# Optimization experiments

Measured on AMD Instinct MI355X. Metric: run time of the kernel, lower is better.

## Reference

```python
import jax, jax.numpy as jnp
import numpy as np

# dims: B=batch, S=src_len, H=hidden, E=char_embed, V=vocab, L=lstm layers
B, S, H, E, V, L = 512, 64, 1024, 256, 128, 2


def setup_inputs() -> dict:
    key = jax.random.key(0)
    ks = jax.random.split(key, 20)
    def n(k, shape, scale=0.05):
        return jax.random.normal(k, shape, dtype=jnp.float32) * scale
    return {
        "input_ids": jax.random.randint(ks[0], (B, 1), 0, V),
        "hidden": n(ks[1], (L, B, H), 1.0),
        "cell": n(ks[2], (L, B, H), 1.0),
        "encoder_outputs": n(ks[3], (B, S, H), 1.0),
        "emb": n(ks[4], (V, E)),          # nn.Embedding weight
        "U": n(ks[5], (H, H)),             # attention U (applied as x @ U)
        "W": n(ks[6], (H, H)),             # attention W
        "Vw": n(ks[7], (H, 1)),            # attention V -> scalar score
        "Wih0": n(ks[8], (4 * H, E + H)),  # LSTM layer0 input weights (i,f,g,o)
        "Whh0": n(ks[9], (4 * H, H)),
        "bih0": n(ks[10], (4 * H,)),
        "bhh0": n(ks[11], (4 * H,)),
        "Wih1": n(ks[12], (4 * H, H)),     # LSTM layer1
        "Whh1": n(ks[13], (4 * H, H)),
        "bih1": n(ks[14], (4 * H,)),
        "bhh1": n(ks[15], (4 * H,)),
        "out_w": n(ks[16], (V, H)),        # output nn.Linear weight (out,in)
        "out_b": n(ks[17], (V,)),
        "matrix": 0,
    }


def _lstm_step(x, h, c, Wih, Whh, bih, bhh):
    g = x @ Wih.T + h @ Whh.T + bih + bhh          # (B, 4H), torch gate order i,f,g,o
    i, f, gg, o = jnp.split(g, 4, axis=-1)
    c2 = jax.nn.sigmoid(f) * c + jax.nn.sigmoid(i) * jnp.tanh(gg)
    h2 = jax.nn.sigmoid(o) * jnp.tanh(c2)
    return h2, c2


def reference(input_ids, hidden, cell, encoder_outputs, emb, U, W, Vw,
              Wih0, Whh0, bih0, bhh0, Wih1, Whh1, bih1, bhh1,
              out_w, out_b, matrix):
    embedded = emb[input_ids]                                  # (B,1,E)
    t1 = jnp.einsum('bsh,hk->bsk', encoder_outputs, U)         # U(enc): (B,S,H)
    t2 = hidden[-1] @ W                                        # W(h_top): (B,H)
    e = jnp.tanh(t1 + t2[:, None, :]) @ Vw                     # scores: (B,S,1)
    a = jax.nn.softmax(e, axis=1)                              # attention weights over S
    ct = jnp.einsum('bso,bsh->boh', a, encoder_outputs)        # context: (B,1,H)
    x = jnp.concatenate([embedded, ct], axis=2)[:, 0, :]       # (B, E+H); dropout p=0 -> identity
    h0, c0 = _lstm_step(x, hidden[0], cell[0], Wih0, Whh0, bih0, bhh0)
    h1, c1 = _lstm_step(h0, hidden[1], cell[1], Wih1, Whh1, bih1, bhh1)
    out = (h1 @ out_w.T + out_b)[:, None, :]                   # (B,1,V)
    h_new = jnp.stack([h0, h1])
    c_new = jnp.stack([c0, c1])
    if matrix:
        return (a, out, h_new, c_new)
    return (out, h_new, c_new)
```

## Files before the change

### kernel.cpp

```cpp
#include <hip/hip_runtime.h>
#include <stdint.h>

#define BB 512
#define SS 64
#define HH 1024
#define EE 256
#define VV 128

typedef __attribute__((ext_vector_type(8))) short bf16x8;
typedef __attribute__((ext_vector_type(4))) float f32x4;

constexpr size_t OFF_ENC   = 0;
constexpr size_t OFF_WIH0  = OFF_ENC   + 67108864UL;
constexpr size_t OFF_WHH0  = OFF_WIH0  + 10485760UL;
constexpr size_t OFF_WIH1  = OFF_WHH0  + 8388608UL;
constexpr size_t OFF_WHH1  = OFF_WIH1  + 8388608UL;
constexpr size_t OFF_OUTW  = OFF_WHH1  + 8388608UL;
constexpr size_t OFF_HID0  = OFF_OUTW  + 262144UL;
constexpr size_t OFF_HLAST = OFF_HID0  + 1048576UL;
constexpr size_t OFF_UT    = OFF_HLAST + 1048576UL;
constexpr size_t OFF_WT    = OFF_UT    + 2097152UL;
constexpr size_t OFF_T2    = OFF_WT    + 2097152UL;
constexpr size_t OFF_E     = OFF_T2    + 2097152UL;
constexpr size_t OFF_EMB   = OFF_E     + 131072UL;
constexpr size_t OFF_CT    = OFF_EMB   + 262144UL;
constexpr size_t OFF_G     = OFF_CT    + 1048576UL;
constexpr size_t OFF_H0B   = OFF_G     + 8388608UL;
constexpr size_t OFF_H1B   = OFF_H0B   + 1048576UL;

__device__ __forceinline__ unsigned short f2bf(float f) {
  unsigned int u = __float_as_uint(f);
  unsigned int r = (u + 0x7FFFu + ((u >> 16) & 1u)) >> 16;
  return (unsigned short)r;
}
__device__ __forceinline__ float bf2f(unsigned short h) {
  return __uint_as_float(((unsigned int)h) << 16);
}

__device__ __forceinline__ void gload_lds16(const void* g, void* l) {
  __builtin_amdgcn_global_load_lds(
      (const __attribute__((address_space(1))) unsigned int*)g,
      (__attribute__((address_space(3))) unsigned int*)l, 16, 0, 0);
}

__global__ void cvt_all(const float* __restrict__ enc, const float* __restrict__ Wih0,
                        const float* __restrict__ Whh0, const float* __restrict__ Wih1,
                        const float* __restrict__ Whh1, const float* __restrict__ outw,
                        const float* __restrict__ hid, char* __restrict__ ws) {
  long i = (long)blockIdx.x * 256 + threadIdx.x;
  const long stride = (long)gridDim.x * 256;
  for (; i < 13139968L; i += stride) {
    const float4* src; ushort4* dst; long j;
    if (i < 8388608L)       { src = (const float4*)enc;  dst = (ushort4*)(ws + OFF_ENC);  j = i; }
    else if (i < 9699328L)  { src = (const float4*)Wih0; dst = (ushort4*)(ws + OFF_WIH0); j = i - 8388608L; }
    else if (i < 10747904L) { src = (const float4*)Whh0; dst = (ushort4*)(ws + OFF_WHH0); j = i - 9699328L; }
    else if (i < 11796480L) { src = (const float4*)Wih1; dst = (ushort4*)(ws + OFF_WIH1); j = i - 10747904L; }
    else if (i < 12845056L) { src = (const float4*)Whh1; dst = (ushort4*)(ws + OFF_WHH1); j = i - 11796480L; }
    else if (i < 12877824L) { src = (const float4*)outw; dst = (ushort4*)(ws + OFF_OUTW); j = i - 12845056L; }
    else if (i < 13008896L) { src = (const float4*)hid;  dst = (ushort4*)(ws + OFF_HID0); j = i - 12877824L; }
    else { src = (const float4*)(hid + 524288); dst = (ushort4*)(ws + OFF_HLAST); j = i - 13008896L; }
    float4 v = src[j];
    ushort4 o;
    o.x = f2bf(v.x); o.y = f2bf(v.y); o.z = f2bf(v.z); o.w = f2bf(v.w);
    dst[j] = o;
  }
}

__global__ void transpose_cvt2(const float* __restrict__ U, const float* __restrict__ W,
                               char* __restrict__ ws) {
  __shared__ float tile[32][33];
  const float* in = blockIdx.z ? W : U;
  unsigned short* out = (unsigned short*)(ws + (blockIdx.z ? OFF_WT : OFF_UT));
  int bc = blockIdx.x * 32, br = blockIdx.y * 32;
  int tx = threadIdx.x & 31, ty = threadIdx.x >> 5;
#pragma unroll
  for (int i = 0; i < 32; i += 8)
    tile[ty + i][tx] = in[(long)(br + ty + i) * HH + bc + tx];
  __syncthreads();
#pragma unroll
  for (int i = 0; i < 32; i += 8)
    out[(long)(bc + ty + i) * HH + br + tx] = f2bf(tile[tx][ty + i]);
}

__global__ void build_xemb(const int* __restrict__ ids, const float* __restrict__ emb,
                           unsigned short* __restrict__ embb) {
  int t = blockIdx.x * 256 + threadIdx.x;
  int b = t >> 6, c4 = t & 63;
  float4 v = ((const float4*)(emb + (long)ids[b] * 256))[c4];
  ushort4 o;
  o.x = f2bf(v.x); o.y = f2bf(v.y); o.z = f2bf(v.z); o.w = f2bf(v.w);
  ((ushort4*)embb)[t] = o;
}

__global__ __launch_bounds__(256) void gemm_seg(
    const unsigned short* __restrict__ A0, int KA0,
    const unsigned short* __restrict__ A1, int KA1,
    const unsigned short* __restrict__ A2,
    const unsigned short* __restrict__ B0, int KB0,
    const unsigned short* __restrict__ B1,
    float* __restrict__ C, int N, int Ktot) {
  __shared__ alignas(128) unsigned short lA[128 * 64];
  __shared__ alignas(128) unsigned short lB[64 * 64];
  const int tid = threadIdx.x;
  const int lane = tid & 63, wid = tid >> 6;
  const int wr = wid >> 1, wc = wid & 1;
  const int fr = lane & 15, fg = lane >> 4;
  f32x4 acc[4][2] = {};
  const long rowA0 = (long)blockIdx.x * 128;
  const long rowB0 = (long)blockIdx.y * 64;
  for (int kt = 0; kt < Ktot; kt += 64) {
    const unsigned short* Ap; int ka, lda;
    if (kt < KA0)            { Ap = A0; ka = kt;             lda = KA0; }
    else if (kt < KA0 + KA1) { Ap = A1; ka = kt - KA0;       lda = KA1; }
    else                     { Ap = A2; ka = kt - KA0 - KA1; lda = 1024; }
    const unsigned short* Bp; int kb, ldb;
    if (kt < KB0) { Bp = B0; kb = kt;       ldb = KB0; }
    else          { Bp = B1; kb = kt - KB0; ldb = 1024; }
#pragma unroll
    for (int j = 0; j < 4; ++j) {
      int c = j * 256 + tid;
      int r = c >> 3, cc = c & 7;
      int sc = cc ^ ((r >> 1) & 7);
      gload_lds16(Ap + (rowA0 + r) * (long)lda + ka + sc * 8, &lA[c * 8]);
    }
#pragma unroll
    for (int j = 0; j < 2; ++j) {
      int c = j * 256 + tid;
      int r = c >> 3, cc = c & 7;
      int sc = cc ^ ((r >> 1) & 7);
      gload_lds16(Bp + (rowB0 + r) * (long)ldb + kb + sc * 8, &lB[c * 8]);
    }
    __syncthreads();
#pragma unroll
    for (int kk = 0; kk < 64; kk += 32) {
      bf16x8 af[4], bfv[2];
#pragma unroll
      for (int m = 0; m < 4; ++m) {
        int row = wr * 64 + m * 16 + fr;
        int ch = ((kk >> 3) + fg) ^ ((row >> 1) & 7);
        af[m] = *(const bf16x8*)&lA[row * 64 + ch * 8];
      }
#pragma unroll
      for (int n = 0; n < 2; ++n) {
        int row = wc * 32 + n * 16 + fr;
        int ch = ((kk >> 3) + fg) ^ ((row >> 1) & 7);
        bfv[n] = *(const bf16x8*)&lB[row * 64 + ch * 8];
      }
#pragma unroll
      for (int m = 0; m < 4; ++m)
#pragma unroll
        for (int n = 0; n < 2; ++n)
          acc[m][n] = __builtin_amdgcn_mfma_f32_16x16x32_bf16(af[m], bfv[n],
                                                              acc[m][n], 0, 0, 0);
    }
    __syncthreads();
  }
#pragma unroll
  for (int m = 0; m < 4; ++m)
#pragma unroll
    for (int n = 0; n < 2; ++n)
#pragma unroll
      for (int r = 0; r < 4; ++r) {
        long grow = rowA0 + wr * 64 + m * 16 + fg * 4 + r;
        long gcol = rowB0 + wc * 32 + n * 16 + fr;
        C[grow * N + gcol] = acc[m][n][r];
      }
}

__global__ __launch_bounds__(256) void gemm_outproj(
    const unsigned short* __restrict__ A, const unsigned short* __restrict__ Bt,
    float* __restrict__ C) {
  __shared__ alignas(128) unsigned short lA[128 * 64];
  __shared__ alignas(128) unsigned short lB[128 * 64];
  const int tid = threadIdx.x;
  const int lane = tid & 63, wid = tid >> 6;
  const int wr = wid >> 1, wc = wid & 1;
  const int fr = lane & 15, fg = lane >> 4;
  f32x4 acc[4][4] = {};
  const long rowA0 = (long)blockIdx.x * 128;
  const int k0 = blockIdx.y * 128;
  for (int kt = k0; kt < k0 + 128; kt += 64) {
#pragma unroll
    for (int j = 0; j < 4; ++j) {
      int c = j * 256 + tid;
      int r = c >> 3, cc = c & 7;
      gload_lds16(A + (rowA0 + r) * 1024 + kt + cc * 8, &lA[c * 8]);
    }
#pragma unroll
    for (int j = 0; j < 4; ++j) {
      int c = j * 256 + tid;
      int r = c >> 3, cc = c & 7;
      gload_lds16(Bt + (long)r * 1024 + kt + cc * 8, &lB[c * 8]);
    }
    __syncthreads();
#pragma unroll
    for (int kk = 0; kk < 64; kk += 32) {
      bf16x8 af[4], bfv[4];
#pragma unroll
      for (int m = 0; m < 4; ++m)
        af[m] = *(const bf16x8*)&lA[(wr * 64 + m * 16 + fr) * 64 + kk + fg * 8];
#pragma unroll
      for (int n = 0; n < 4; ++n)
        bfv[n] = *(const bf16x8*)&lB[(wc * 64 + n * 16 + fr) * 64 + kk + fg * 8];
#pragma unroll
      for (int m = 0; m < 4; ++m)
#pragma unroll
        for (int n = 0; n < 4; ++n)
          acc[m][n] = __builtin_amdgcn_mfma_f32_16x16x32_bf16(af[m], bfv[n],
                                                              acc[m][n], 0, 0, 0);
    }
    __syncthreads();
  }
#pragma unroll
  for (int m = 0; m < 4; ++m)
#pragma unroll
    for (int n = 0; n < 4; ++n)
#pragma unroll
      for (int r = 0; r < 4; ++r) {
        long grow = rowA0 + wr * 64 + m * 16 + fg * 4 + r;
        long gcol = wc * 64 + n * 16 + fr;
        atomicAdd(&C[grow * 128 + gcol], acc[m][n][r]);
      }
}

__global__ void init_out_bias(const float* __restrict__ ob, float* __restrict__ out) {
  int i = blockIdx.x * 256 + threadIdx.x;
  out[i] = ob[i & 127];
}

__global__ __launch_bounds__(512, 2) void gemm_score256(
    const unsigned short* __restrict__ A, const unsigned short* __restrict__ Bt,
    const float* __restrict__ t2, const float* __restrict__ Vw,
    float* __restrict__ e) {
  extern __shared__ unsigned short smem[];
  const int K = HH;
  const int tid = threadIdx.x;
  const int lane = tid & 63, wid = tid >> 6;
  const int wr = wid >> 2;
  const int wcc = wid & 3;
  const int fr = lane & 15, fg = lane >> 4;
  int flat = blockIdx.y * 4 + blockIdx.x;
  int swz = (flat & 7) * 64 + (flat >> 3);
  const long rowA0 = (long)(swz >> 2) * 256;
  const long rowB0 = (long)(swz & 3) * 256;
  const int NKT = 16, NIT = 8;

  f32x4 acc[8][4] = {};

  auto RA = [&](int buf, int kh) { return (const unsigned short*)(smem + (buf * 4 + kh * 2) * 8192); };
  auto RB = [&](int buf, int kh) { return (const unsigned short*)(smem + (buf * 4 + kh * 2 + 1) * 8192); };

  auto stage = [&](int buf, int reg, int ktile) {
    const unsigned short* base = (reg & 1) ? Bt : A;
    long r0 = (reg & 1) ? rowB0 : rowA0;
    int kb = ktile * 64 + (reg >> 1) * 32;
    unsigned short* dst = smem + (buf * 4 + reg) * 8192;
#pragma unroll
    for (int j = 0; j < 2; ++j) {
      int c = j * 512 + tid;
      int row = c >> 2;
      int fgl = (c & 3) ^ ((row >> 1) & 3);
      gload_lds16(base + (r0 + row) * (long)K + kb + fgl * 8, dst + c * 8);
    }
  };
  auto readA = [&](const unsigned short* rg, int mh, bf16x8* af) {
#pragma unroll
    for (int m = 0; m < 4; ++m) {
      int row = wr * 128 + mh * 64 + m * 16 + fr;
      int slot = fg ^ ((row >> 1) & 3);
      af[m] = *(const bf16x8*)(rg + row * 32 + slot * 8);
    }
  };
  auto readB = [&](const unsigned short* rg, bf16x8* bv) {
#pragma unroll
    for (int n = 0; n < 4; ++n) {
      int row = wcc * 64 + n * 16 + fr;
      int slot = fg ^ ((row >> 1) & 3);
      bv[n] = *(const bf16x8*)(rg + row * 32 + slot * 8);
    }
  };
  auto mfma16 = [&](int mh, const bf16x8* af, const bf16x8* bv) {
    __builtin_amdgcn_s_setprio(1);
#pragma unroll
    for (int m = 0; m < 4; ++m)
#pragma unroll
      for (int n = 0; n < 4; ++n)
        acc[mh * 4 + m][n] = __builtin_amdgcn_mfma_f32_16x16x32_bf16(
            af[m], bv[n], acc[mh * 4 + m][n], 0, 0, 0);
    __builtin_amdgcn_s_setprio(0);
  };

#define BAR() __builtin_amdgcn_s_barrier()
#define WAIT6() asm volatile("s_waitcnt vmcnt(6)" ::: "memory")

  bf16x8 afA[4], afB[4], bvA[4], bvB[4];

  stage(0, 0, 0); stage(0, 1, 0); stage(0, 2, 0); stage(0, 3, 0);
  stage(1, 0, 1); stage(1, 1, 1);
  asm volatile("s_waitcnt vmcnt(8)" ::: "memory");
  BAR();
  readA(RA(0, 0), 0, afA); readB(RB(0, 0), bvA);

  for (int t = 0; t < NIT; ++t) {
    int k1 = 2 * t + 1, k2 = 2 * t + 2, k3 = 2 * t + 3;
    if (k2 >= NKT) k2 -= NKT;
    if (k3 >= NKT) k3 -= NKT;
    readA(RA(0, 0), 1, afB);
    stage(1, 2, k1);
    BAR(); mfma16(0, afA, bvA); BAR();
    WAIT6();
    readA(RA(0, 1), 0, afA); readB(RB(0, 1), bvB);
    stage(1, 3, k1);
    BAR(); mfma16(1, afB, bvA); BAR();
    readA(RA(0, 1), 1, afB);
    stage(0, 0, k2);
    BAR(); mfma16(0, afA, bvB); BAR();
    WAIT6();
    readA(RA(1, 0), 0, afA); readB(RB(1, 0), bvA);
    stage(0, 1, k2);
    BAR(); mfma16(1, afB, bvB); BAR();
    readA(RA(1, 0), 1, afB);
    stage(0, 2, k2);
    BAR(); mfma16(0, afA, bvA); BAR();
    WAIT6();
    readA(RA(1, 1), 0, afA); readB(RB(1, 1), bvB);
    stage(0, 3, k2);
    BAR(); mfma16(1, afB, bvA); BAR();
    readA(RA(1, 1), 1, afB);
    stage(1, 0, k3);
    BAR(); mfma16(0, afA, bvB); BAR();
    WAIT6();
    readA(RA(0, 0), 0, afA); readB(RB(0, 0), bvA);
    stage(1, 1, k3);
    BAR(); mfma16(1, afB, bvB); BAR();
  }
  asm volatile("s_waitcnt vmcnt(0)" ::: "memory");

  float t2v[2][4], vw[4];
#pragma unroll
  for (int n = 0; n < 4; ++n) {
    long col = rowB0 + wcc * 64 + n * 16 + fr;
    vw[n] = Vw[col];
#pragma unroll
    for (int h = 0; h < 2; ++h) {
      long b = (rowA0 >> 6) + wr * 2 + h;
      t2v[h][n] = t2[b * HH + col];
    }
  }
#pragma unroll
  for (int i = 0; i < 8; ++i) {
    int hsel = i >> 2;
    float part[4] = {0.f, 0.f, 0.f, 0.f};
#pragma unroll
    for (int n = 0; n < 4; ++n) {
#pragma unroll
      for (int r = 0; r < 4; ++r) {
        float tval = acc[i][n][r] + t2v[hsel][n];
        float th = 1.f - 2.f / (__expf(2.f * tval) + 1.f);
        part[r] += th * vw[n];
      }
    }
#pragma unroll
    for (int r = 0; r < 4; ++r) {
      float p = part[r];
      p += __shfl_xor(p, 1);
      p += __shfl_xor(p, 2);
      p += __shfl_xor(p, 4);
      p += __shfl_xor(p, 8);
      if (fr == 0)
        atomicAdd(&e[rowA0 + wr * 128 + i * 16 + fg * 4 + r], p);
    }
  }
#undef BAR
#undef WAIT6
}

__global__ void softmax_ctx(const float* __restrict__ e,
                            const unsigned short* __restrict__ encb,
                            unsigned short* __restrict__ ctb) {
  __shared__ float als[2][64];
  const int tid = threadIdx.x;
  const int bpair = blockIdx.x;
  if (tid < 128) {
    int b = bpair * 2 + (tid >> 6), s = tid & 63;
    float v = e[b * 64 + s];
    float mx = v;
#pragma unroll
    for (int o = 32; o; o >>= 1) mx = fmaxf(mx, __shfl_xor(mx, o));
    float ex = __expf(v - mx);
    float sm = ex;
#pragma unroll
    for (int o = 32; o; o >>= 1) sm += __shfl_xor(sm, o);
    als[tid >> 6][s] = ex / sm;
  }
  __syncthreads();
  int bi = tid >> 7, hg = tid & 127;
  int b = bpair * 2 + bi;
  const unsigned short* er = encb + (long)b * (SS * HH) + hg * 8;
  float s[8] = {0.f, 0.f, 0.f, 0.f, 0.f, 0.f, 0.f, 0.f};
  for (int i = 0; i < 64; ++i) {
    float av = als[bi][i];
    bf16x8 v = *(const bf16x8*)(er + (long)i * HH);
#pragma unroll
    for (int j = 0; j < 8; ++j) s[j] += av * bf2f((unsigned short)v[j]);
  }
  unsigned short* dst = ctb + (long)b * HH + hg * 8;
#pragma unroll
  for (int j = 0; j < 8; ++j) dst[j] = f2bf(s[j]);
}

__global__ void lstm_cell(const float* __restrict__ g, const float* __restrict__ bih,
                          const float* __restrict__ bhh, const float* __restrict__ cin,
                          float* __restrict__ hout, float* __restrict__ cout,
                          unsigned short* __restrict__ hb) {
  int idx = blockIdx.x * 256 + threadIdx.x;
  int b = idx >> 10, h = idx & 1023;
  const float* gr = g + (long)b * 4096;
  float gi = gr[h] + bih[h] + bhh[h];
  float gf = gr[1024 + h] + bih[1024 + h] + bhh[1024 + h];
  float gg = gr[2048 + h] + bih[2048 + h] + bhh[2048 + h];
  float go = gr[3072 + h] + bih[3072 + h] + bhh[3072 + h];
  float si = 1.f / (1.f + __expf(-gi));
  float sf = 1.f / (1.f + __expf(-gf));
  float so = 1.f / (1.f + __expf(-go));
  float tg = 1.f - 2.f / (__expf(2.f * gg) + 1.f);
  float c2 = sf * cin[idx] + si * tg;
  float tc = 1.f - 2.f / (__expf(2.f * c2) + 1.f);
  float h2 = so * tc;
  cout[idx] = c2;
  hout[idx] = h2;
  hb[idx] = f2bf(h2);
}

extern "C" void kernel_launch(void* const* d_in, const int* in_sizes, int n_in,
                              void* d_out, int out_size, void* d_ws, size_t ws_size,
                              hipStream_t stream) {
  const int* ids = (const int*)d_in[0];
  const float* hidden = (const float*)d_in[1];
  const float* cell = (const float*)d_in[2];
  const float* enc = (const float*)d_in[3];
  const float* emb = (const float*)d_in[4];
  const float* U = (const float*)d_in[5];
  const float* W = (const float*)d_in[6];
  const float* Vw = (const float*)d_in[7];
  const float* Wih0 = (const float*)d_in[8];
  const float* Whh0 = (const float*)d_in[9];
  const float* bih0 = (const float*)d_in[10];
  const float* bhh0 = (const float*)d_in[11];
  const float* Wih1 = (const float*)d_in[12];
  const float* Whh1 = (const float*)d_in[13];
  const float* bih1 = (const float*)d_in[14];
  const float* bhh1 = (const float*)d_in[15];
  const float* out_w = (const float*)d_in[16];
  const float* out_b = (const float*)d_in[17];
  float* out = (float*)d_out;
  char* ws = (char*)d_ws;
  (void)in_sizes; (void)n_in; (void)out_size; (void)ws_size;

  unsigned short* enc_b  = (unsigned short*)(ws + OFF_ENC);
  unsigned short* Wih0b  = (unsigned short*)(ws + OFF_WIH0);
  unsigned short* Whh0b  = (unsigned short*)(ws + OFF_WHH0);
  unsigned short* Wih1b  = (unsigned short*)(ws + OFF_WIH1);
  unsigned short* Whh1b  = (unsigned short*)(ws + OFF_WHH1);
  unsigned short* outwb  = (unsigned short*)(ws + OFF_OUTW);
  unsigned short* hid0b  = (unsigned short*)(ws + OFF_HID0);
  unsigned short* hlastb = (unsigned short*)(ws + OFF_HLAST);
  unsigned short* Utb    = (unsigned short*)(ws + OFF_UT);
  unsigned short* Wtb    = (unsigned short*)(ws + OFF_WT);
  float*          t2     = (float*)(ws + OFF_T2);
  float*          e      = (float*)(ws + OFF_E);
  unsigned short* embb   = (unsigned short*)(ws + OFF_EMB);
  unsigned short* ctb    = (unsigned short*)(ws + OFF_CT);
  float*          g      = (float*)(ws + OFF_G);
  unsigned short* h0b    = (unsigned short*)(ws + OFF_H0B);
  unsigned short* h1b    = (unsigned short*)(ws + OFF_H1B);

  float* out_logits = out;
  float* h_new = out + BB * VV;
  float* c_new = h_new + 2 * BB * HH;

  cvt_all<<<2048, 256, 0, stream>>>(enc, Wih0, Whh0, Wih1, Whh1, out_w, hidden, ws);
  transpose_cvt2<<<dim3(32, 32, 2), 256, 0, stream>>>(U, W, ws);
  build_xemb<<<128, 256, 0, stream>>>(ids, emb, embb);
  hipMemsetAsync(e, 0, (size_t)BB * SS * 4, stream);

  gemm_seg<<<dim3(4, 16), 256, 0, stream>>>(hlastb, 1024, nullptr, 0, nullptr,
                                            Wtb, 1024, nullptr, t2, HH, 1024);

  (void)hipFuncSetAttribute(reinterpret_cast<const void*>(gemm_score256),
                            hipFuncAttributeMaxDynamicSharedMemorySize, 131072);
  gemm_score256<<<dim3(4, 128), 512, 131072, stream>>>(enc_b, Utb, t2, Vw, e);

  softmax_ctx<<<256, 256, 0, stream>>>(e, enc_b, ctb);

  gemm_seg<<<dim3(4, 64), 256, 0, stream>>>(embb, 256, ctb, 1024, hid0b,
                                            Wih0b, 1280, Whh0b, g, 4 * HH, 2304);
  lstm_cell<<<BB * HH / 256, 256, 0, stream>>>(g, bih0, bhh0, cell, h_new, c_new, h0b);

  gemm_seg<<<dim3(4, 64), 256, 0, stream>>>(h0b, 1024, hlastb, 1024, nullptr,
                                            Wih1b, 1024, Whh1b, g, 4 * HH, 2048);
  lstm_cell<<<BB * HH / 256, 256, 0, stream>>>(g, bih1, bhh1, cell + BB * HH,
                                               h_new + BB * HH, c_new + BB * HH, h1b);

  init_out_bias<<<BB * VV / 256, 256, 0, stream>>>(out_b, out_logits);
  gemm_outproj<<<dim3(4, 8), 256, 0, stream>>>(h1b, outwb, out_logits);
}
```

Before: 256.9 us.

## Split LSTM gate GEMMs along K into two partial buffers; widen conversion kernel

The LSTM gate GEMMs now run with a z-dimension of two, each half covering half the K range and writing its partial sum to its own buffer (the second reuses the encoder region of the workspace, which is no longer needed at that point). lstm_cell adds the two partial sums. This doubles block count from 256 to 512 so more CUs are busy. The cost is extra partial-sum traffic and a dependence on the encoder buffer being dead by then. The fp32-to-bf16 conversion kernel also now processes eight elements per unit with four units in flight per thread, to raise memory-level parallelism.

```diff
diff --git a/kernel.cpp b/kernel.cpp
--- a/kernel.cpp
+++ b/kernel.cpp
@@ -9,6 +9,7 @@
 
 typedef __attribute__((ext_vector_type(8))) short bf16x8;
 typedef __attribute__((ext_vector_type(4))) float f32x4;
+typedef __attribute__((ext_vector_type(8))) unsigned short u16x8;
 
 constexpr size_t OFF_ENC   = 0;
 constexpr size_t OFF_WIH0  = OFF_ENC   + 67108864UL;
@@ -43,26 +44,58 @@
       (__attribute__((address_space(3))) unsigned int*)l, 16, 0, 0);
 }
 
-__global__ void cvt_all(const float* __restrict__ enc, const float* __restrict__ Wih0,
-                        const float* __restrict__ Whh0, const float* __restrict__ Wih1,
-                        const float* __restrict__ Whh1, const float* __restrict__ outw,
-                        const float* __restrict__ hid, char* __restrict__ ws) {
-  long i = (long)blockIdx.x * 256 + threadIdx.x;
-  const long stride = (long)gridDim.x * 256;
-  for (; i < 13139968L; i += stride) {
-    const float4* src; ushort4* dst; long j;
-    if (i < 8388608L)       { src = (const float4*)enc;  dst = (ushort4*)(ws + OFF_ENC);  j = i; }
-    else if (i < 9699328L)  { src = (const float4*)Wih0; dst = (ushort4*)(ws + OFF_WIH0); j = i - 8388608L; }
-    else if (i < 10747904L) { src = (const float4*)Whh0; dst = (ushort4*)(ws + OFF_WHH0); j = i - 9699328L; }
-    else if (i < 11796480L) { src = (const float4*)Wih1; dst = (ushort4*)(ws + OFF_WIH1); j = i - 10747904L; }
-    else if (i < 12845056L) { src = (const float4*)Whh1; dst = (ushort4*)(ws + OFF_WHH1); j = i - 11796480L; }
-    else if (i < 12877824L) { src = (const float4*)outw; dst = (ushort4*)(ws + OFF_OUTW); j = i - 12845056L; }
-    else if (i < 13008896L) { src = (const float4*)hid;  dst = (ushort4*)(ws + OFF_HID0); j = i - 12877824L; }
-    else { src = (const float4*)(hid + 524288); dst = (ushort4*)(ws + OFF_HLAST); j = i - 13008896L; }
-    float4 v = src[j];
-    ushort4 o;
-    o.x = f2bf(v.x); o.y = f2bf(v.y); o.z = f2bf(v.z); o.w = f2bf(v.w);
-    dst[j] = o;
+constexpr long CU0 = 4194304;
+constexpr long CU1 = CU0 + 655360;
+constexpr long CU2 = CU1 + 524288;
+constexpr long CU3 = CU2 + 524288;
+constexpr long CU4 = CU3 + 524288;
+constexpr long CU5 = CU4 + 16384;
+constexpr long CU6 = CU5 + 65536;
+constexpr long CU7 = CU6 + 65536;
+
+__global__ void cvt_fast(const float* __restrict__ enc, const float* __restrict__ Wih0,
+                         const float* __restrict__ Whh0, const float* __restrict__ Wih1,
+                         const float* __restrict__ Whh1, const float* __restrict__ outw,
+                         const float* __restrict__ hid, char* __restrict__ ws) {
+  auto resolve = [&](long u, const float4*& s, u16x8*& d) {
+    long j;
+    if (u < CU0)      { j = u;       s = (const float4*)enc  + 2 * j; d = (u16x8*)(ws + OFF_ENC)   + j; }
+    else if (u < CU1) { j = u - CU0; s = (const float4*)Wih0 + 2 * j; d = (u16x8*)(ws + OFF_WIH0)  + j; }
+    else if (u < CU2) { j = u - CU1; s = (const float4*)Whh0 + 2 * j; d = (u16x8*)(ws + OFF_WHH0)  + j; }
+    else if (u < CU3) { j = u - CU2; s = (const float4*)Wih1 + 2 * j; d = (u16x8*)(ws + OFF_WIH1)  + j; }
+    else if (u < CU4) { j = u - CU3; s = (const float4*)Whh1 + 2 * j; d = (u16x8*)(ws + OFF_WHH1)  + j; }
+    else if (u < CU5) { j = u - CU4; s = (const float4*)outw + 2 * j; d = (u16x8*)(ws + OFF_OUTW)  + j; }
+    else if (u < CU6) { j = u - CU5; s = (const float4*)hid  + 2 * j; d = (u16x8*)(ws + OFF_HID0)  + j; }
+    else              { j = u - CU6; s = (const float4*)(hid + 524288) + 2 * j; d = (u16x8*)(ws + OFF_HLAST) + j; }
+  };
+  const long T = (long)gridDim.x * blockDim.x;
+  long t = (long)blockIdx.x * blockDim.x + threadIdx.x;
+  for (long base = t; base < CU7; base += 4 * T) {
+    long u1 = base + T, u2 = base + 2 * T, u3 = base + 3 * T;
+    bool a1 = u1 < CU7, a2 = u2 < CU7, a3 = u3 < CU7;
+    const float4 *s0, *s1, *s2, *s3;
+    u16x8 *d0, *d1, *d2, *d3;
+    resolve(base, s0, d0);
+    resolve(a1 ? u1 : base, s1, d1);
+    resolve(a2 ? u2 : base, s2, d2);
+    resolve(a3 ? u3 : base, s3, d3);
+    float4 v00 = s0[0], v01 = s0[1];
+    float4 v10 = s1[0], v11 = s1[1];
+    float4 v20 = s2[0], v21 = s2[1];
+    float4 v30 = s3[0], v31 = s3[1];
+    u16x8 o0, o1, o2, o3;
+    o0[0] = f2bf(v00.x); o0[1] = f2bf(v00.y); o0[2] = f2bf(v00.z); o0[3] = f2bf(v00.w);
+    o0[4] = f2bf(v01.x); o0[5] = f2bf(v01.y); o0[6] = f2bf(v01.z); o0[7] = f2bf(v01.w);
+    o1[0] = f2bf(v10.x); o1[1] = f2bf(v10.y); o1[2] = f2bf(v10.z); o1[3] = f2bf(v10.w);
+    o1[4] = f2bf(v11.x); o1[5] = f2bf(v11.y); o1[6] = f2bf(v11.z); o1[7] = f2bf(v11.w);
+    o2[0] = f2bf(v20.x); o2[1] = f2bf(v20.y); o2[2] = f2bf(v20.z); o2[3] = f2bf(v20.w);
+    o2[4] = f2bf(v21.x); o2[5] = f2bf(v21.y); o2[6] = f2bf(v21.z); o2[7] = f2bf(v21.w);
+    o3[0] = f2bf(v30.x); o3[1] = f2bf(v30.y); o3[2] = f2bf(v30.z); o3[3] = f2bf(v30.w);
+    o3[4] = f2bf(v31.x); o3[5] = f2bf(v31.y); o3[6] = f2bf(v31.z); o3[7] = f2bf(v31.w);
+    *d0 = o0;
+    if (a1) *d1 = o1;
+    if (a2) *d2 = o2;
+    if (a3) *d3 = o3;
   }
 }
 
@@ -98,7 +131,7 @@
     const unsigned short* __restrict__ A2,
     const unsigned short* __restrict__ B0, int KB0,
     const unsigned short* __restrict__ B1,
-    float* __restrict__ C, int N, int Ktot) {
+    float* __restrict__ C0p, float* __restrict__ C1p, int N, int Ktot, int Khalf) {
   __shared__ alignas(128) unsigned short lA[128 * 64];
   __shared__ alignas(128) unsigned short lB[64 * 64];
   const int tid = threadIdx.x;
@@ -108,7 +141,10 @@
   f32x4 acc[4][2] = {};
   const long rowA0 = (long)blockIdx.x * 128;
   const long rowB0 = (long)blockIdx.y * 64;
-  for (int kt = 0; kt < Ktot; kt += 64) {
+  const int ktb = blockIdx.z * Khalf;
+  int kte = ktb + Khalf; if (kte > Ktot) kte = Ktot;
+  float* C = blockIdx.z ? C1p : C0p;
+  for (int kt = ktb; kt < kte; kt += 64) {
     const unsigned short* Ap; int ka, lda;
     if (kt < KA0)            { Ap = A0; ka = kt;             lda = KA0; }
     else if (kt < KA0 + KA1) { Ap = A1; ka = kt - KA0;       lda = KA1; }
@@ -409,17 +445,19 @@
   for (int j = 0; j < 8; ++j) dst[j] = f2bf(s[j]);
 }
 
-__global__ void lstm_cell(const float* __restrict__ g, const float* __restrict__ bih,
-                          const float* __restrict__ bhh, const float* __restrict__ cin,
+__global__ void lstm_cell(const float* __restrict__ g0, const float* __restrict__ g1,
+                          const float* __restrict__ bih, const float* __restrict__ bhh,
+                          const float* __restrict__ cin,
                           float* __restrict__ hout, float* __restrict__ cout,
                           unsigned short* __restrict__ hb) {
   int idx = blockIdx.x * 256 + threadIdx.x;
   int b = idx >> 10, h = idx & 1023;
-  const float* gr = g + (long)b * 4096;
-  float gi = gr[h] + bih[h] + bhh[h];
-  float gf = gr[1024 + h] + bih[1024 + h] + bhh[1024 + h];
-  float gg = gr[2048 + h] + bih[2048 + h] + bhh[2048 + h];
-  float go = gr[3072 + h] + bih[3072 + h] + bhh[3072 + h];
+  const float* gr0 = g0 + (long)b * 4096;
+  const float* gr1 = g1 + (long)b * 4096;
+  float gi = gr0[h] + gr1[h] + bih[h] + bhh[h];
+  float gf = gr0[1024 + h] + gr1[1024 + h] + bih[1024 + h] + bhh[1024 + h];
+  float gg = gr0[2048 + h] + gr1[2048 + h] + bih[2048 + h] + bhh[2048 + h];
+  float go = gr0[3072 + h] + gr1[3072 + h] + bih[3072 + h] + bhh[3072 + h];
   float si = 1.f / (1.f + __expf(-gi));
   float sf = 1.f / (1.f + __expf(-gf));
   float so = 1.f / (1.f + __expf(-go));
@@ -472,6 +510,7 @@
   unsigned short* embb   = (unsigned short*)(ws + OFF_EMB);
   unsigned short* ctb    = (unsigned short*)(ws + OFF_CT);
   float*          g      = (float*)(ws + OFF_G);
+  float*          gB     = (float*)(ws + OFF_ENC);
   unsigned short* h0b    = (unsigned short*)(ws + OFF_H0B);
   unsigned short* h1b    = (unsigned short*)(ws + OFF_H1B);
 
@@ -479,13 +518,13 @@
   float* h_new = out + BB * VV;
   float* c_new = h_new + 2 * BB * HH;
 
-  cvt_all<<<2048, 256, 0, stream>>>(enc, Wih0, Whh0, Wih1, Whh1, out_w, hidden, ws);
+  cvt_fast<<<2048, 256, 0, stream>>>(enc, Wih0, Whh0, Wih1, Whh1, out_w, hidden, ws);
   transpose_cvt2<<<dim3(32, 32, 2), 256, 0, stream>>>(U, W, ws);
   build_xemb<<<128, 256, 0, stream>>>(ids, emb, embb);
   hipMemsetAsync(e, 0, (size_t)BB * SS * 4, stream);
 
-  gemm_seg<<<dim3(4, 16), 256, 0, stream>>>(hlastb, 1024, nullptr, 0, nullptr,
-                                            Wtb, 1024, nullptr, t2, HH, 1024);
+  gemm_seg<<<dim3(4, 16, 1), 256, 0, stream>>>(hlastb, 1024, nullptr, 0, nullptr,
+                                               Wtb, 1024, nullptr, t2, t2, HH, 1024, 1024);
 
   (void)hipFuncSetAttribute(reinterpret_cast<const void*>(gemm_score256),
                             hipFuncAttributeMaxDynamicSharedMemorySize, 131072);
@@ -493,13 +532,13 @@
 
   softmax_ctx<<<256, 256, 0, stream>>>(e, enc_b, ctb);
 
-  gemm_seg<<<dim3(4, 64), 256, 0, stream>>>(embb, 256, ctb, 1024, hid0b,
-                                            Wih0b, 1280, Whh0b, g, 4 * HH, 2304);
-  lstm_cell<<<BB * HH / 256, 256, 0, stream>>>(g, bih0, bhh0, cell, h_new, c_new, h0b);
-
-  gemm_seg<<<dim3(4, 64), 256, 0, stream>>>(h0b, 1024, hlastb, 1024, nullptr,
-                                            Wih1b, 1024, Whh1b, g, 4 * HH, 2048);
-  lstm_cell<<<BB * HH / 256, 256, 0, stream>>>(g, bih1, bhh1, cell + BB * HH,
+  gemm_seg<<<dim3(4, 64, 2), 256, 0, stream>>>(embb, 256, ctb, 1024, hid0b,
+                                               Wih0b, 1280, Whh0b, g, gB, 4 * HH, 2304, 1152);
+  lstm_cell<<<BB * HH / 256, 256, 0, stream>>>(g, gB, bih0, bhh0, cell, h_new, c_new, h0b);
+
+  gemm_seg<<<dim3(4, 64, 2), 256, 0, stream>>>(h0b, 1024, hlastb, 1024, nullptr,
+                                               Wih1b, 1024, Whh1b, g, gB, 4 * HH, 2048, 1024);
+  lstm_cell<<<BB * HH / 256, 256, 0, stream>>>(g, gB, bih1, bhh1, cell + BB * HH,
                                                h_new + BB * HH, c_new + BB * HH, h1b);
 
   init_out_bias<<<BB * VV / 256, 256, 0, stream>>>(out_b, out_logits);
```

Measured after the change: 237.5 us. 7.5% less time.

## Fuse fp32-to-bf16 conversion into GEMM loads and split LSTM GEMMs along K

Applied to the files above, without the earlier changes.

Removes the bulk pre-conversion pass over encoder outputs and LSTM weights. The score GEMM now loads fp32 encoder rows into registers, converts them and writes bf16 into LDS inside a simpler double-buffered loop. The LSTM GEMMs read fp32 weights and convert them while staging. softmax_ctx reads fp32 encoder outputs directly. LSTM GEMMs are split into two K halves writing separate partial buffers that lstm_cell sums, which doubles the grid for occupancy. The cost is more global bytes per GEMM load and conversion work inside the GEMM loops.

```diff
diff --git a/kernel.cpp b/kernel.cpp
--- a/kernel.cpp
+++ b/kernel.cpp
@@ -9,13 +9,10 @@
 
 typedef __attribute__((ext_vector_type(8))) short bf16x8;
 typedef __attribute__((ext_vector_type(4))) float f32x4;
-
-constexpr size_t OFF_ENC   = 0;
-constexpr size_t OFF_WIH0  = OFF_ENC   + 67108864UL;
-constexpr size_t OFF_WHH0  = OFF_WIH0  + 10485760UL;
-constexpr size_t OFF_WIH1  = OFF_WHH0  + 8388608UL;
-constexpr size_t OFF_WHH1  = OFF_WIH1  + 8388608UL;
-constexpr size_t OFF_OUTW  = OFF_WHH1  + 8388608UL;
+typedef __attribute__((ext_vector_type(8))) unsigned short u16x8;
+
+constexpr size_t OFF_SCRATCH = 0;
+constexpr size_t OFF_OUTW  = OFF_SCRATCH + 67108864UL;
 constexpr size_t OFF_HID0  = OFF_OUTW  + 262144UL;
 constexpr size_t OFF_HLAST = OFF_HID0  + 1048576UL;
 constexpr size_t OFF_UT    = OFF_HLAST + 1048576UL;
@@ -43,27 +40,19 @@
       (__attribute__((address_space(3))) unsigned int*)l, 16, 0, 0);
 }
 
-__global__ void cvt_all(const float* __restrict__ enc, const float* __restrict__ Wih0,
-                        const float* __restrict__ Whh0, const float* __restrict__ Wih1,
-                        const float* __restrict__ Whh1, const float* __restrict__ outw,
-                        const float* __restrict__ hid, char* __restrict__ ws) {
-  long i = (long)blockIdx.x * 256 + threadIdx.x;
-  const long stride = (long)gridDim.x * 256;
-  for (; i < 13139968L; i += stride) {
-    const float4* src; ushort4* dst; long j;
-    if (i < 8388608L)       { src = (const float4*)enc;  dst = (ushort4*)(ws + OFF_ENC);  j = i; }
-    else if (i < 9699328L)  { src = (const float4*)Wih0; dst = (ushort4*)(ws + OFF_WIH0); j = i - 8388608L; }
-    else if (i < 10747904L) { src = (const float4*)Whh0; dst = (ushort4*)(ws + OFF_WHH0); j = i - 9699328L; }
-    else if (i < 11796480L) { src = (const float4*)Wih1; dst = (ushort4*)(ws + OFF_WIH1); j = i - 10747904L; }
-    else if (i < 12845056L) { src = (const float4*)Whh1; dst = (ushort4*)(ws + OFF_WHH1); j = i - 11796480L; }
-    else if (i < 12877824L) { src = (const float4*)outw; dst = (ushort4*)(ws + OFF_OUTW); j = i - 12845056L; }
-    else if (i < 13008896L) { src = (const float4*)hid;  dst = (ushort4*)(ws + OFF_HID0); j = i - 12877824L; }
-    else { src = (const float4*)(hid + 524288); dst = (ushort4*)(ws + OFF_HLAST); j = i - 13008896L; }
-    float4 v = src[j];
-    ushort4 o;
-    o.x = f2bf(v.x); o.y = f2bf(v.y); o.z = f2bf(v.z); o.w = f2bf(v.w);
-    dst[j] = o;
-  }
+__global__ __launch_bounds__(256) void cvt_small(const float* __restrict__ hid,
+                                                 const float* __restrict__ outw,
+                                                 char* __restrict__ ws) {
+  int i = blockIdx.x * 256 + threadIdx.x;
+  const float4* src;
+  ushort4* dst;
+  int j;
+  if (i < 262144) { src = (const float4*)hid;  dst = (ushort4*)(ws + OFF_HID0); j = i; }
+  else            { src = (const float4*)outw; dst = (ushort4*)(ws + OFF_OUTW); j = i - 262144; }
+  float4 v = src[j];
+  ushort4 o;
+  o.x = f2bf(v.x); o.y = f2bf(v.y); o.z = f2bf(v.z); o.w = f2bf(v.w);
+  dst[j] = o;
 }
 
 __global__ void transpose_cvt2(const float* __restrict__ U, const float* __restrict__ W,
@@ -92,13 +81,13 @@
   ((ushort4*)embb)[t] = o;
 }
 
+template <int BF32>
 __global__ __launch_bounds__(256) void gemm_seg(
     const unsigned short* __restrict__ A0, int KA0,
     const unsigned short* __restrict__ A1, int KA1,
     const unsigned short* __restrict__ A2,
-    const unsigned short* __restrict__ B0, int KB0,
-    const unsigned short* __restrict__ B1,
-    float* __restrict__ C, int N, int Ktot) {
+    const void* __restrict__ B0v, int KB0, const void* __restrict__ B1v,
+    float* __restrict__ C0p, float* __restrict__ C1p, int N, int Ktot, int Khalf) {
   __shared__ alignas(128) unsigned short lA[128 * 64];
   __shared__ alignas(128) unsigned short lB[64 * 64];
   const int tid = threadIdx.x;
@@ -108,27 +97,55 @@
   f32x4 acc[4][2] = {};
   const long rowA0 = (long)blockIdx.x * 128;
   const long rowB0 = (long)blockIdx.y * 64;
-  for (int kt = 0; kt < Ktot; kt += 64) {
+  const int ktb = blockIdx.z * Khalf;
+  int kte = ktb + Khalf; if (kte > Ktot) kte = Ktot;
+  float* C = blockIdx.z ? C1p : C0p;
+  for (int kt = ktb; kt < kte; kt += 64) {
     const unsigned short* Ap; int ka, lda;
     if (kt < KA0)            { Ap = A0; ka = kt;             lda = KA0; }
     else if (kt < KA0 + KA1) { Ap = A1; ka = kt - KA0;       lda = KA1; }
     else                     { Ap = A2; ka = kt - KA0 - KA1; lda = 1024; }
-    const unsigned short* Bp; int kb, ldb;
-    if (kt < KB0) { Bp = B0; kb = kt;       ldb = KB0; }
-    else          { Bp = B1; kb = kt - KB0; ldb = 1024; }
-#pragma unroll
-    for (int j = 0; j < 4; ++j) {
-      int c = j * 256 + tid;
-      int r = c >> 3, cc = c & 7;
-      int sc = cc ^ ((r >> 1) & 7);
-      gload_lds16(Ap + (rowA0 + r) * (long)lda + ka + sc * 8, &lA[c * 8]);
-    }
-#pragma unroll
-    for (int j = 0; j < 2; ++j) {
-      int c = j * 256 + tid;
-      int r = c >> 3, cc = c & 7;
-      int sc = cc ^ ((r >> 1) & 7);
-      gload_lds16(Bp + (rowB0 + r) * (long)ldb + kb + sc * 8, &lB[c * 8]);
+    if constexpr (BF32) {
+      const float* Bp; int kb, ldb;
+      if (kt < KB0) { Bp = (const float*)B0v; kb = kt;       ldb = KB0; }
+      else          { Bp = (const float*)B1v; kb = kt - KB0; ldb = 1024; }
+      const int brow = tid >> 2, bkq = tid & 3;
+      const f32x4* bs = (const f32x4*)(Bp + (rowB0 + brow) * (long)ldb + kb) + bkq * 4;
+      f32x4 q0 = bs[0], q1 = bs[1], q2 = bs[2], q3 = bs[3];
+#pragma unroll
+      for (int j = 0; j < 4; ++j) {
+        int c = j * 256 + tid;
+        int r = c >> 3, cc = c & 7;
+        int sc = cc ^ ((r >> 1) & 7);
+        gload_lds16(Ap + (rowA0 + r) * (long)lda + ka + sc * 8, &lA[c * 8]);
+      }
+      const int bx = (brow >> 1) & 7;
+      u16x8 w0, w1;
+#pragma unroll
+      for (int j = 0; j < 4; ++j) {
+        w0[j] = f2bf(q0[j]); w0[4 + j] = f2bf(q1[j]);
+        w1[j] = f2bf(q2[j]); w1[4 + j] = f2bf(q3[j]);
+      }
+      *(u16x8*)&lB[brow * 64 + (((bkq * 2) ^ bx) * 8)] = w0;
+      *(u16x8*)&lB[brow * 64 + (((bkq * 2 + 1) ^ bx) * 8)] = w1;
+    } else {
+      const unsigned short* Bp; int kb, ldb;
+      if (kt < KB0) { Bp = (const unsigned short*)B0v; kb = kt;       ldb = KB0; }
+      else          { Bp = (const unsigned short*)B1v; kb = kt - KB0; ldb = 1024; }
+#pragma unroll
+      for (int j = 0; j < 4; ++j) {
+        int c = j * 256 + tid;
+        int r = c >> 3, cc = c & 7;
+        int sc = cc ^ ((r >> 1) & 7);
+        gload_lds16(Ap + (rowA0 + r) * (long)lda + ka + sc * 8, &lA[c * 8]);
+      }
+#pragma unroll
+      for (int j = 0; j < 2; ++j) {
+        int c = j * 256 + tid;
+        int r = c >> 3, cc = c & 7;
+        int sc = cc ^ ((r >> 1) & 7);
+        gload_lds16(Bp + (rowB0 + r) * (long)ldb + kb + sc * 8, &lB[c * 8]);
+      }
     }
     __syncthreads();
 #pragma unroll
@@ -229,11 +246,10 @@
 }
 
 __global__ __launch_bounds__(512, 2) void gemm_score256(
-    const unsigned short* __restrict__ A, const unsigned short* __restrict__ Bt,
+    const float* __restrict__ Af, const unsigned short* __restrict__ Bt,
     const float* __restrict__ t2, const float* __restrict__ Vw,
     float* __restrict__ e) {
   extern __shared__ unsigned short smem[];
-  const int K = HH;
   const int tid = threadIdx.x;
   const int lane = tid & 63, wid = tid >> 6;
   const int wr = wid >> 2;
@@ -243,27 +259,45 @@
   int swz = (flat & 7) * 64 + (flat >> 3);
   const long rowA0 = (long)(swz >> 2) * 256;
   const long rowB0 = (long)(swz & 3) * 256;
-  const int NKT = 16, NIT = 8;
 
   f32x4 acc[8][4] = {};
 
-  auto RA = [&](int buf, int kh) { return (const unsigned short*)(smem + (buf * 4 + kh * 2) * 8192); };
-  auto RB = [&](int buf, int kh) { return (const unsigned short*)(smem + (buf * 4 + kh * 2 + 1) * 8192); };
-
-  auto stage = [&](int buf, int reg, int ktile) {
-    const unsigned short* base = (reg & 1) ? Bt : A;
-    long r0 = (reg & 1) ? rowB0 : rowA0;
-    int kb = ktile * 64 + (reg >> 1) * 32;
-    unsigned short* dst = smem + (buf * 4 + reg) * 8192;
-#pragma unroll
-    for (int j = 0; j < 2; ++j) {
-      int c = j * 512 + tid;
-      int row = c >> 2;
-      int fgl = (c & 3) ^ ((row >> 1) & 3);
-      gload_lds16(base + (r0 + row) * (long)K + kb + fgl * 8, dst + c * 8);
-    }
+  const int arow = tid >> 1, akh = tid & 1;
+  const float* ag = Af + (rowA0 + arow) * 1024 + akh * 32;
+  const int awx = (arow >> 1) & 3;
+  f32x4 areg[8];
+
+  auto issueA = [&](int kt) {
+    const f32x4* p = (const f32x4*)(ag + kt * 64);
+#pragma unroll
+    for (int j = 0; j < 8; ++j) areg[j] = p[j];
   };
-  auto readA = [&](const unsigned short* rg, int mh, bf16x8* af) {
+  auto writeA = [&](int buf) {
+    unsigned short* wb = smem + buf * 32768 + akh * 8192 + arow * 32;
+#pragma unroll
+    for (int s = 0; s < 4; ++s) {
+      u16x8 o;
+#pragma unroll
+      for (int q = 0; q < 8; ++q) o[q] = f2bf(areg[s * 2 + (q >> 2)][q & 3]);
+      *(u16x8*)(wb + ((s ^ awx) * 8)) = o;
+    }
+  };
+  auto stageB = [&](int buf, int kt) {
+#pragma unroll
+    for (int kh = 0; kh < 2; ++kh) {
+      unsigned short* dst = smem + buf * 32768 + (2 + kh) * 8192;
+      int kb = kt * 64 + kh * 32;
+#pragma unroll
+      for (int j = 0; j < 2; ++j) {
+        int c = j * 512 + tid;
+        int row = c >> 2;
+        int fgl = (c & 3) ^ ((row >> 1) & 3);
+        gload_lds16(Bt + (rowB0 + row) * 1024L + kb + fgl * 8, dst + c * 8);
+      }
+    }
+  };
+  auto readA4 = [&](int buf, int kh, int mh, bf16x8* af) {
+    const unsigned short* rg = smem + buf * 32768 + kh * 8192;
 #pragma unroll
     for (int m = 0; m < 4; ++m) {
       int row = wr * 128 + mh * 64 + m * 16 + fr;
@@ -271,7 +305,8 @@
       af[m] = *(const bf16x8*)(rg + row * 32 + slot * 8);
     }
   };
-  auto readB = [&](const unsigned short* rg, bf16x8* bv) {
+  auto readB4 = [&](int buf, int kh, bf16x8* bv) {
+    const unsigned short* rg = smem + buf * 32768 + (2 + kh) * 8192;
 #pragma unroll
     for (int n = 0; n < 4; ++n) {
       int row = wcc * 64 + n * 16 + fr;
@@ -290,49 +325,35 @@
     __builtin_amdgcn_s_setprio(0);
   };
 
-#define BAR() __builtin_amdgcn_s_barrier()
-#define WAIT6() asm volatile("s_waitcnt vmcnt(6)" ::: "memory")
-
-  bf16x8 afA[4], afB[4], bvA[4], bvB[4];
-
-  stage(0, 0, 0); stage(0, 1, 0); stage(0, 2, 0); stage(0, 3, 0);
-  stage(1, 0, 1); stage(1, 1, 1);
+  issueA(0);
+  stageB(0, 0);
+  asm volatile("s_waitcnt vmcnt(4)" ::: "memory");
+  writeA(0);
+  issueA(1);
+  asm volatile("s_waitcnt lgkmcnt(0)" ::: "memory");
   asm volatile("s_waitcnt vmcnt(8)" ::: "memory");
-  BAR();
-  readA(RA(0, 0), 0, afA); readB(RB(0, 0), bvA);
-
-  for (int t = 0; t < NIT; ++t) {
-    int k1 = 2 * t + 1, k2 = 2 * t + 2, k3 = 2 * t + 3;
-    if (k2 >= NKT) k2 -= NKT;
-    if (k3 >= NKT) k3 -= NKT;
-    readA(RA(0, 0), 1, afB);
-    stage(1, 2, k1);
-    BAR(); mfma16(0, afA, bvA); BAR();
-    WAIT6();
-    readA(RA(0, 1), 0, afA); readB(RB(0, 1), bvB);
-    stage(1, 3, k1);
-    BAR(); mfma16(1, afB, bvA); BAR();
-    readA(RA(0, 1), 1, afB);
-    stage(0, 0, k2);
-    BAR(); mfma16(0, afA, bvB); BAR();
-    WAIT6();
-    readA(RA(1, 0), 0, afA); readB(RB(1, 0), bvA);
-    stage(0, 1, k2);
-    BAR(); mfma16(1, afB, bvB); BAR();
-    readA(RA(1, 0), 1, afB);
-    stage(0, 2, k2);
-    BAR(); mfma16(0, afA, bvA); BAR();
-    WAIT6();
-    readA(RA(1, 1), 0, afA); readB(RB(1, 1), bvB);
-    stage(0, 3, k2);
-    BAR(); mfma16(1, afB, bvA); BAR();
-    readA(RA(1, 1), 1, afB);
-    stage(1, 0, k3);
-    BAR(); mfma16(0, afA, bvB); BAR();
-    WAIT6();
-    readA(RA(0, 0), 0, afA); readB(RB(0, 0), bvA);
-    stage(1, 1, k3);
-    BAR(); mfma16(1, afB, bvB); BAR();
+  __builtin_amdgcn_s_barrier();
+
+#pragma unroll 2
+  for (int u = 0; u < 16; ++u) {
+    const int cur = u & 1, nxt = cur ^ 1;
+    stageB(nxt, (u + 1) & 15);
+    bf16x8 af[4], bv[4];
+    readB4(cur, 0, bv);
+    readA4(cur, 0, 0, af);
+    mfma16(0, af, bv);
+    readA4(cur, 0, 1, af);
+    mfma16(1, af, bv);
+    writeA(nxt);
+    issueA((u + 2) & 15);
+    readB4(cur, 1, bv);
+    readA4(cur, 1, 0, af);
+    mfma16(0, af, bv);
+    readA4(cur, 1, 1, af);
+    asm volatile("s_waitcnt lgkmcnt(0)" ::: "memory");
+    mfma16(1, af, bv);
+    asm volatile("s_waitcnt vmcnt(8)" ::: "memory");
+    __builtin_amdgcn_s_barrier();
   }
   asm volatile("s_waitcnt vmcnt(0)" ::: "memory");
 
@@ -371,12 +392,10 @@
         atomicAdd(&e[rowA0 + wr * 128 + i * 16 + fg * 4 + r], p);
     }
   }
-#undef BAR
-#undef WAIT6
 }
 
 __global__ void softmax_ctx(const float* __restrict__ e,
-                            const unsigned short* __restrict__ encb,
+                            const float* __restrict__ enc,
                             unsigned short* __restrict__ ctb) {
   __shared__ float als[2][64];
   const int tid = threadIdx.x;
@@ -396,30 +415,33 @@
   __syncthreads();
   int bi = tid >> 7, hg = tid & 127;
   int b = bpair * 2 + bi;
-  const unsigned short* er = encb + (long)b * (SS * HH) + hg * 8;
+  const float* er = enc + (long)b * (SS * HH) + hg * 8;
   float s[8] = {0.f, 0.f, 0.f, 0.f, 0.f, 0.f, 0.f, 0.f};
   for (int i = 0; i < 64; ++i) {
     float av = als[bi][i];
-    bf16x8 v = *(const bf16x8*)(er + (long)i * HH);
-#pragma unroll
-    for (int j = 0; j < 8; ++j) s[j] += av * bf2f((unsigned short)v[j]);
+    f32x4 v0 = *(const f32x4*)(er + (long)i * HH);
+    f32x4 v1 = *(const f32x4*)(er + (long)i * HH + 4);
+#pragma unroll
+    for (int j = 0; j < 4; ++j) { s[j] += av * v0[j]; s[4 + j] += av * v1[j]; }
   }
   unsigned short* dst = ctb + (long)b * HH + hg * 8;
 #pragma unroll
   for (int j = 0; j < 8; ++j) dst[j] = f2bf(s[j]);
 }
 
-__global__ void lstm_cell(const float* __restrict__ g, const float* __restrict__ bih,
-                          const float* __restrict__ bhh, const float* __restrict__ cin,
+__global__ void lstm_cell(const float* __restrict__ g0, const float* __restrict__ g1,
+                          const float* __restrict__ bih, const float* __restrict__ bhh,
+                          const float* __restrict__ cin,
                           float* __restrict__ hout, float* __restrict__ cout,
                           unsigned short* __restrict__ hb) {
   int idx = blockIdx.x * 256 + threadIdx.x;
   int b = idx >> 10, h = idx & 1023;
-  const float* gr = g + (long)b * 4096;
-  float gi = gr[h] + bih[h] + bhh[h];
-  float gf = gr[1024 + h] + bih[1024 + h] + bhh[1024 + h];
-  float gg = gr[2048 + h] + bih[2048 + h] + bhh[2048 + h];
-  float go = gr[3072 + h] + bih[3072 + h] + bhh[3072 + h];
+  const float* gr0 = g0 + (long)b * 4096;
+  const float* gr1 = g1 + (long)b * 4096;
+  float gi = gr0[h] + gr1[h] + bih[h] + bhh[h];
+  float gf = gr0[1024 + h] + gr1[1024 + h] + bih[1024 + h] + bhh[1024 + h];
+  float gg = gr0[2048 + h] + gr1[2048 + h] + bih[2048 + h] + bhh[2048 + h];
+  float go = gr0[3072 + h] + gr1[3072 + h] + bih[3072 + h] + bhh[3072 + h];
   float si = 1.f / (1.f + __expf(-gi));
   float sf = 1.f / (1.f + __expf(-gf));
   float so = 1.f / (1.f + __expf(-go));
@@ -457,11 +479,6 @@
   char* ws = (char*)d_ws;
   (void)in_sizes; (void)n_in; (void)out_size; (void)ws_size;
 
-  unsigned short* enc_b  = (unsigned short*)(ws + OFF_ENC);
-  unsigned short* Wih0b  = (unsigned short*)(ws + OFF_WIH0);
-  unsigned short* Whh0b  = (unsigned short*)(ws + OFF_WHH0);
-  unsigned short* Wih1b  = (unsigned short*)(ws + OFF_WIH1);
-  unsigned short* Whh1b  = (unsigned short*)(ws + OFF_WHH1);
   unsigned short* outwb  = (unsigned short*)(ws + OFF_OUTW);
   unsigned short* hid0b  = (unsigned short*)(ws + OFF_HID0);
   unsigned short* hlastb = (unsigned short*)(ws + OFF_HLAST);
@@ -472,6 +489,7 @@
   unsigned short* embb   = (unsigned short*)(ws + OFF_EMB);
   unsigned short* ctb    = (unsigned short*)(ws + OFF_CT);
   float*          g      = (float*)(ws + OFF_G);
+  float*          gB     = (float*)(ws + OFF_SCRATCH);
   unsigned short* h0b    = (unsigned short*)(ws + OFF_H0B);
   unsigned short* h1b    = (unsigned short*)(ws + OFF_H1B);
 
@@ -479,27 +497,27 @@
   float* h_new = out + BB * VV;
   float* c_new = h_new + 2 * BB * HH;
 
-  cvt_all<<<2048, 256, 0, stream>>>(enc, Wih0, Whh0, Wih1, Whh1, out_w, hidden, ws);
+  cvt_small<<<1152, 256, 0, stream>>>(hidden, out_w, ws);
   transpose_cvt2<<<dim3(32, 32, 2), 256, 0, stream>>>(U, W, ws);
   build_xemb<<<128, 256, 0, stream>>>(ids, emb, embb);
   hipMemsetAsync(e, 0, (size_t)BB * SS * 4, stream);
 
-  gemm_seg<<<dim3(4, 16), 256, 0, stream>>>(hlastb, 1024, nullptr, 0, nullptr,
-                                            Wtb, 1024, nullptr, t2, HH, 1024);
+  gemm_seg<0><<<dim3(4, 16, 1), 256, 0, stream>>>(hlastb, 1024, nullptr, 0, nullptr,
+                                                  Wtb, 1024, nullptr, t2, t2, HH, 1024, 1024);
 
   (void)hipFuncSetAttribute(reinterpret_cast<const void*>(gemm_score256),
                             hipFuncAttributeMaxDynamicSharedMemorySize, 131072);
-  gemm_score256<<<dim3(4, 128), 512, 131072, stream>>>(enc_b, Utb, t2, Vw, e);
-
-  softmax_ctx<<<256, 256, 0, stream>>>(e, enc_b, ctb);
-
-  gemm_seg<<<dim3(4, 64), 256, 0, stream>>>(embb, 256, ctb, 1024, hid0b,
-                                            Wih0b, 1280, Whh0b, g, 4 * HH, 2304);
-  lstm_cell<<<BB * HH / 256, 256, 0, stream>>>(g, bih0, bhh0, cell, h_new, c_new, h0b);
-
-  gemm_seg<<<dim3(4, 64), 256, 0, stream>>>(h0b, 1024, hlastb, 1024, nullptr,
-                                            Wih1b, 1024, Whh1b, g, 4 * HH, 2048);
-  lstm_cell<<<BB * HH / 256, 256, 0, stream>>>(g, bih1, bhh1, cell + BB * HH,
+  gemm_score256<<<dim3(4, 128), 512, 131072, stream>>>(enc, Utb, t2, Vw, e);
+
+  softmax_ctx<<<256, 256, 0, stream>>>(e, enc, ctb);
+
+  gemm_seg<1><<<dim3(4, 64, 2), 256, 0, stream>>>(embb, 256, ctb, 1024, hid0b,
+                                                  Wih0, 1280, Whh0, g, gB, 4 * HH, 2304, 1152);
+  lstm_cell<<<BB * HH / 256, 256, 0, stream>>>(g, gB, bih0, bhh0, cell, h_new, c_new, h0b);
+
+  gemm_seg<1><<<dim3(4, 64, 2), 256, 0, stream>>>(h0b, 1024, hlastb, 1024, nullptr,
+                                                  Wih1, 1024, Whh1, g, gB, 4 * HH, 2048, 1024);
+  lstm_cell<<<BB * HH / 256, 256, 0, stream>>>(g, gB, bih1, bhh1, cell + BB * HH,
                                                h_new + BB * HH, c_new + BB * HH, h1b);
 
   init_out_bias<<<BB * VV / 256, 256, 0, stream>>>(out_b, out_logits);
```

Result: slower. 370.7 us (+44.3%).
